# Kernel tuning notes

Measured on AMD Instinct MI355X. Metric: run time of the kernel, lower is better.

## Reference

```python
import jax, jax.numpy as jnp
import numpy as np

N, M, D = 16384, 16384, 16
MAX_NORM = 0.7  # keep points strictly inside Poincare ball

def _to_ball(v):
    # rescale so every point has norm < MAX_NORM
    n = jnp.linalg.norm(v, axis=1, keepdims=True)
    return MAX_NORM * v / (1.0 + n)

def setup_inputs() -> dict:
    key = jax.random.key(0)
    k1, k2 = jax.random.split(key)
    set1 = _to_ball(jax.random.normal(k1, (N, D), dtype=jnp.float32))
    set2 = _to_ball(jax.random.normal(k2, (M, D), dtype=jnp.float32))
    return {"set1": set1, "set2": set2}

def hypcdist(x, y, epsilon=0.0):
    # ||x_i - y_j||^2 for all pairs: [N, M]
    diff = x[:, None, :] - y[None, :, :]
    sqdist = jnp.sum(diff * diff, axis=-1)
    x_norm = jnp.sum(x * x, axis=1)[:, None]   # [N,1]
    y_norm = jnp.sum(y * y, axis=1)[None, :]   # [1,M]
    u = 1.0 + 2.0 * sqdist / ((1.0 - x_norm) * (1.0 - y_norm)) + epsilon
    v = jnp.sqrt(u * u - 1.0)
    return jnp.log(u + v)  # arcosh(u)

def reference(set1, set2):
    d2 = hypcdist(set1, set2)                 # [N, M]
    term_1 = jnp.mean(jnp.min(d2, axis=1))    # for each point in set1, nearest in set2
    term_2 = jnp.mean(jnp.min(d2, axis=0))    # for each point in set2, nearest in set1
    return term_1 + term_2                    # directed=False
```

## Files before the change

kernel.cpp:

```cpp
#include <hip/hip_runtime.h>
#include <math.h>

#define NPTS 16384
#define DIM  16
#define KH   32
#define CSPLIT 16
#define COLS_PER_BLOCK (NPTS / CSPLIT)
#define JT_TOTAL (COLS_PER_BLOCK / 16)
#define ROWS_PER_BLOCK 512
#define RBLK (NPTS / ROWS_PER_BLOCK)
#define MT 8
#define NBLOCKS (RBLK * CSPLIT)

typedef _Float16 f16x8 __attribute__((ext_vector_type(8)));
typedef float    f32x4 __attribute__((ext_vector_type(4)));

__global__ __launch_bounds__(256) void prep_kernel(const float* __restrict__ s1,
                                                   const float* __restrict__ s2,
                                                   _Float16* __restrict__ Xa,
                                                   _Float16* __restrict__ Yb,
                                                   unsigned int* __restrict__ rowfinal,
                                                   float* __restrict__ out) {
    int b = blockIdx.x, tid = threadIdx.x;
    int idx = b * 256 + tid;
    rowfinal[idx] = 0xFFFFFFFFu;
    if (idx == 0) out[0] = 0.f;

    int isX = (b < 64);
    const float* src = isX ? s1 : s2;
    _Float16* dst = isX ? Xa : Yb;
    int p = (isX ? b : b - 64) * 256 + tid;

    const float4* s4 = (const float4*)(src + (size_t)p * DIM);
    float4 A = s4[0], B = s4[1], C = s4[2], D = s4[3];
    float v[DIM] = {A.x,A.y,A.z,A.w, B.x,B.y,B.z,B.w,
                    C.x,C.y,C.z,C.w, D.x,D.y,D.z,D.w};
    float n2 = 0.f;
#pragma unroll
    for (int k = 0; k < DIM; ++k) n2 = fmaf(v[k], v[k], n2);
    float r = 1.0f / (1.0f - n2);

    __attribute__((aligned(16))) _Float16 buf[KH];
#pragma unroll
    for (int k = 0; k < DIM; ++k) buf[k] = (_Float16)(r * v[k]);
    if (isX) { buf[16] = (_Float16)(0.5f * r * n2);  buf[17] = (_Float16)r; }
    else     { buf[16] = (_Float16)(-r);             buf[17] = (_Float16)(-0.5f * r * n2); }
#pragma unroll
    for (int k = 18; k < KH; ++k) buf[k] = (_Float16)0.f;

    int g = p >> 4, c = p & 15;
    const uint4* b4 = (const uint4*)buf;
#pragma unroll
    for (int q = 0; q < 4; ++q) {
        size_t off = (size_t)g * 512 + (size_t)q * 128 + (size_t)c * 8;
        *(uint4*)(dst + off) = b4[q];
    }
}

__global__ __launch_bounds__(256, 2) void pairs_kernel(const _Float16* __restrict__ Xa,
                                                       const _Float16* __restrict__ Yb,
                                                       unsigned int* __restrict__ rowfinal) {
    __shared__ __align__(16) _Float16 Bs[COLS_PER_BLOCK * KH];
    __shared__ unsigned int colLDS[COLS_PER_BLOCK];

    const int b = blockIdx.x;
    const int r  = b >> 4;
    const int cs = b & 15;

    unsigned int* colfinal = rowfinal + NPTS;

    const int tid = threadIdx.x;
    const int lane = tid & 63, w = tid >> 6;
    const int c = lane & 15, quad = lane >> 4;

    {
        const char* gsrc = (const char*)Yb + (size_t)cs * (COLS_PER_BLOCK * KH * 2)
                         + (size_t)tid * 16;
        char* lb = (char*)Bs + (size_t)tid * 16;
#pragma unroll
        for (int e = 0; e < 16; ++e) {
            __builtin_amdgcn_global_load_lds(
                (const __attribute__((address_space(1))) unsigned int*)(gsrc + e * 4096),
                (__attribute__((address_space(3))) unsigned int*)(lb + e * 4096),
                16, 0, 0);
        }
    }
#pragma unroll
    for (int e = 0; e < 4; ++e) colLDS[tid + e * 256] = 0xFFFFFFFFu;

    f16x8 af[MT];
#pragma unroll
    for (int t = 0; t < MT; ++t) {
        int g = r * 32 + w * 8 + t;
        af[t] = *(const f16x8*)&Xa[(size_t)g * 512 + (size_t)lane * 8];
    }

    f32x4 rowmax[MT];
#pragma unroll
    for (int t = 0; t < MT; ++t)
        rowmax[t] = (f32x4){-INFINITY, -INFINITY, -INFINITY, -INFINITY};

    const f32x4 zero = (f32x4){0.f, 0.f, 0.f, 0.f};

    __syncthreads();

#pragma unroll 2
    for (int jt = 0; jt < JT_TOTAL; ++jt) {
        f16x8 bf = *(const f16x8*)&Bs[jt * 512 + lane * 8];
        float cm = -INFINITY;
#pragma unroll
        for (int t = 0; t < MT; ++t) {
            f32x4 acc = __builtin_amdgcn_mfma_f32_16x16x32_f16(af[t], bf, zero, 0, 0, 0);
            rowmax[t][0] = fmaxf(rowmax[t][0], acc[0]);
            rowmax[t][1] = fmaxf(rowmax[t][1], acc[1]);
            rowmax[t][2] = fmaxf(rowmax[t][2], acc[2]);
            rowmax[t][3] = fmaxf(rowmax[t][3], acc[3]);
            float cv = fmaxf(fmaxf(acc[0], acc[1]), fmaxf(acc[2], acc[3]));
            cm = fmaxf(cm, cv);
        }
        cm = fmaxf(cm, __shfl_xor(cm, 16, 64));
        cm = fmaxf(cm, __shfl_xor(cm, 32, 64));
        if (quad == 0)
            atomicMin(&colLDS[jt * 16 + c], __float_as_uint(cm));
    }

#pragma unroll
    for (int t = 0; t < MT; ++t) {
#pragma unroll
        for (int e = 0; e < 4; ++e) {
            float m = rowmax[t][e];
            m = fmaxf(m, __shfl_xor(m, 1, 64));
            m = fmaxf(m, __shfl_xor(m, 2, 64));
            m = fmaxf(m, __shfl_xor(m, 4, 64));
            m = fmaxf(m, __shfl_xor(m, 8, 64));
            if (c == 0) {
                int row = ((r * 32 + w * 8 + t) << 4) + quad * 4 + e;
                atomicMin(&rowfinal[row], __float_as_uint(m));
            }
        }
    }

    __syncthreads();
#pragma unroll
    for (int e = 0; e < 4; ++e) {
        int i = tid + e * 256;
        atomicMin(&colfinal[cs * COLS_PER_BLOCK + i], colLDS[i]);
    }
}

__global__ __launch_bounds__(256) void finalize_kernel(const unsigned int* __restrict__ rowfinal,
                                                       float* __restrict__ out) {
    int idx = blockIdx.x * 256 + threadIdx.x;
    float f = __uint_as_float(rowfinal[idx]);
    float t = fmaxf(-4.0f * f, 0.0f);
    float d = log1pf(t + sqrtf(t * (t + 2.0f)));
    float val = d * (1.0f / NPTS);

    __shared__ float sred[256];
    sred[threadIdx.x] = val;
    __syncthreads();
    for (int s = 128; s > 0; s >>= 1) {
        if (threadIdx.x < s) sred[threadIdx.x] += sred[threadIdx.x + s];
        __syncthreads();
    }
    if (threadIdx.x == 0) atomicAdd(out, sred[0]);
}

extern "C" void kernel_launch(void* const* d_in, const int* in_sizes, int n_in,
                              void* d_out, int out_size, void* d_ws, size_t ws_size,
                              hipStream_t stream) {
    const float* set1 = (const float*)d_in[0];
    const float* set2 = (const float*)d_in[1];
    float* out = (float*)d_out;

    _Float16* Xa = (_Float16*)d_ws;
    _Float16* Yb = Xa + (size_t)NPTS * KH;
    unsigned int* rowfinal = (unsigned int*)(Yb + (size_t)NPTS * KH);

    prep_kernel<<<128, 256, 0, stream>>>(set1, set2, Xa, Yb, rowfinal, out);
    pairs_kernel<<<NBLOCKS, 256, 0, stream>>>(Xa, Yb, rowfinal);
    finalize_kernel<<<2 * NPTS / 256, 256, 0, stream>>>(rowfinal, out);
}
```

Baseline: 93.92 us.

## Fuse finalize into pairs kernel via last-block reduction and double column split

Doubles the column split so each block handles 512 columns, giving 1024 blocks and a smaller LDS footprint. Replaces the per-tile LDS atomicMin on column minima with plain per-wave stores followed by a 4-way min after the barrier. Removes the separate finalize kernel: a global counter identifies the last block, which then computes the arcosh values and the mean. This saves a launch and some LDS atomics, at the cost of twice as many global column atomics, re-loading A fragments per block, and a serial single-block final reduction.

```diff
diff --git a/kernel.cpp b/kernel.cpp
--- a/kernel.cpp
+++ b/kernel.cpp
@@ -4,7 +4,7 @@
 #define NPTS 16384
 #define DIM  16
 #define KH   32
-#define CSPLIT 16
+#define CSPLIT 32
 #define COLS_PER_BLOCK (NPTS / CSPLIT)
 #define JT_TOTAL (COLS_PER_BLOCK / 16)
 #define ROWS_PER_BLOCK 512
@@ -20,11 +20,11 @@
                                                    _Float16* __restrict__ Xa,
                                                    _Float16* __restrict__ Yb,
                                                    unsigned int* __restrict__ rowfinal,
-                                                   float* __restrict__ out) {
+                                                   unsigned int* __restrict__ counter) {
     int b = blockIdx.x, tid = threadIdx.x;
     int idx = b * 256 + tid;
     rowfinal[idx] = 0xFFFFFFFFu;
-    if (idx == 0) out[0] = 0.f;
+    if (idx == 0) *counter = 0u;
 
     int isX = (b < 64);
     const float* src = isX ? s1 : s2;
@@ -59,15 +59,15 @@
 
 __global__ __launch_bounds__(256, 2) void pairs_kernel(const _Float16* __restrict__ Xa,
                                                        const _Float16* __restrict__ Yb,
-                                                       unsigned int* __restrict__ rowfinal) {
+                                                       unsigned int* __restrict__ rowfinal,
+                                                       unsigned int* __restrict__ counter,
+                                                       float* __restrict__ out) {
     __shared__ __align__(16) _Float16 Bs[COLS_PER_BLOCK * KH];
-    __shared__ unsigned int colLDS[COLS_PER_BLOCK];
+    __shared__ unsigned int colWave[4][COLS_PER_BLOCK];
 
     const int b = blockIdx.x;
-    const int r  = b >> 4;
-    const int cs = b & 15;
-
-    unsigned int* colfinal = rowfinal + NPTS;
+    const int r  = b >> 5;
+    const int cs = b & 31;
 
     const int tid = threadIdx.x;
     const int lane = tid & 63, w = tid >> 6;
@@ -78,15 +78,13 @@
                          + (size_t)tid * 16;
         char* lb = (char*)Bs + (size_t)tid * 16;
 #pragma unroll
-        for (int e = 0; e < 16; ++e) {
+        for (int e = 0; e < 8; ++e) {
             __builtin_amdgcn_global_load_lds(
                 (const __attribute__((address_space(1))) unsigned int*)(gsrc + e * 4096),
                 (__attribute__((address_space(3))) unsigned int*)(lb + e * 4096),
                 16, 0, 0);
         }
     }
-#pragma unroll
-    for (int e = 0; e < 4; ++e) colLDS[tid + e * 256] = 0xFFFFFFFFu;
 
     f16x8 af[MT];
 #pragma unroll
@@ -121,7 +119,7 @@
         cm = fmaxf(cm, __shfl_xor(cm, 16, 64));
         cm = fmaxf(cm, __shfl_xor(cm, 32, 64));
         if (quad == 0)
-            atomicMin(&colLDS[jt * 16 + c], __float_as_uint(cm));
+            colWave[w][jt * 16 + c] = __float_as_uint(cm);
     }
 
 #pragma unroll
@@ -142,28 +140,43 @@
 
     __syncthreads();
 #pragma unroll
-    for (int e = 0; e < 4; ++e) {
+    for (int e = 0; e < 2; ++e) {
         int i = tid + e * 256;
-        atomicMin(&colfinal[cs * COLS_PER_BLOCK + i], colLDS[i]);
+        unsigned int m0 = colWave[0][i], m1 = colWave[1][i];
+        unsigned int m2 = colWave[2][i], m3 = colWave[3][i];
+        unsigned int m01 = m0 < m1 ? m0 : m1;
+        unsigned int m23 = m2 < m3 ? m2 : m3;
+        unsigned int mm  = m01 < m23 ? m01 : m23;
+        atomicMin(&rowfinal[NPTS + cs * COLS_PER_BLOCK + i], mm);
     }
-}
 
-__global__ __launch_bounds__(256) void finalize_kernel(const unsigned int* __restrict__ rowfinal,
-                                                       float* __restrict__ out) {
-    int idx = blockIdx.x * 256 + threadIdx.x;
-    float f = __uint_as_float(rowfinal[idx]);
-    float t = fmaxf(-4.0f * f, 0.0f);
-    float d = log1pf(t + sqrtf(t * (t + 2.0f)));
-    float val = d * (1.0f / NPTS);
-
-    __shared__ float sred[256];
-    sred[threadIdx.x] = val;
+    __threadfence();
+    __shared__ int isLast;
+    if (tid == 0) {
+        unsigned int old = __hip_atomic_fetch_add(counter, 1u, __ATOMIC_ACQ_REL,
+                                                  __HIP_MEMORY_SCOPE_AGENT);
+        isLast = (old == NBLOCKS - 1);
+    }
     __syncthreads();
-    for (int s = 128; s > 0; s >>= 1) {
-        if (threadIdx.x < s) sred[threadIdx.x] += sred[threadIdx.x + s];
+    if (isLast) {
+        float sum = 0.f;
+        for (int k = 0; k < (2 * NPTS) / 256; ++k) {
+            int i = tid + k * 256;
+            unsigned int ub = __hip_atomic_load(&rowfinal[i], __ATOMIC_RELAXED,
+                                                __HIP_MEMORY_SCOPE_AGENT);
+            float f = __uint_as_float(ub);
+            float t = fmaxf(-4.0f * f, 0.0f);
+            sum += log1pf(t + sqrtf(t * (t + 2.0f)));
+        }
+        __shared__ float sred[256];
+        sred[tid] = sum;
         __syncthreads();
+        for (int s = 128; s > 0; s >>= 1) {
+            if (tid < s) sred[tid] += sred[tid + s];
+            __syncthreads();
+        }
+        if (tid == 0) out[0] = sred[0] * (1.0f / NPTS);
     }
-    if (threadIdx.x == 0) atomicAdd(out, sred[0]);
 }
 
 extern "C" void kernel_launch(void* const* d_in, const int* in_sizes, int n_in,
@@ -176,8 +189,8 @@
     _Float16* Xa = (_Float16*)d_ws;
     _Float16* Yb = Xa + (size_t)NPTS * KH;
     unsigned int* rowfinal = (unsigned int*)(Yb + (size_t)NPTS * KH);
+    unsigned int* counter = rowfinal + 2 * NPTS;
 
-    prep_kernel<<<128, 256, 0, stream>>>(set1, set2, Xa, Yb, rowfinal, out);
-    pairs_kernel<<<NBLOCKS, 256, 0, stream>>>(Xa, Yb, rowfinal);
-    finalize_kernel<<<2 * NPTS / 256, 256, 0, stream>>>(rowfinal, out);
+    prep_kernel<<<128, 256, 0, stream>>>(set1, set2, Xa, Yb, rowfinal, counter);
+    pairs_kernel<<<NBLOCKS, 256, 0, stream>>>(Xa, Yb, rowfinal, counter, out);
 }
```

New measurement: 230.2 us. 145% more time.
